# Kernel optimization log

Hardware: AMD Instinct MI355X
Metric: run time of the kernel (lower is better)

Reference implementation:

```python
import jax, jax.numpy as jnp
import numpy as np

B, IN, H, NC = 8192, 1024, 1024, 16
CS = H // NC  # chunk_size = 64


def cumsoftmax(x):
    # cumulative softmax along last dim
    return jnp.cumsum(jax.nn.softmax(x, axis=-1), axis=-1)


def setup_inputs() -> dict:
    key = jax.random.key(0)
    ks = jax.random.split(key, 9)
    s_ih = 1.0 / np.sqrt(IN)
    s_hh = 1.0 / np.sqrt(H)
    return {
        "x": jax.random.normal(ks[0], (B, IN), jnp.float32),
        "hx": jax.random.normal(ks[1], (B, H), jnp.float32),
        "cx": jax.random.normal(ks[2], (B, NC, CS), jnp.float32),
        "input_floor": jax.random.normal(ks[3], (B, NC), jnp.float32),
        "forget_floor": jax.random.normal(ks[4], (B, NC), jnp.float32),
        "W_ih": jax.random.uniform(ks[5], (4 * H, IN), jnp.float32, -s_ih, s_ih),
        "b_ih": jax.random.uniform(ks[6], (4 * H,), jnp.float32, -s_ih, s_ih),
        "W_hh": jax.random.uniform(ks[7], (4 * H, H), jnp.float32, -s_hh, s_hh),
        "b_hh": jax.random.uniform(ks[8], (4 * H,), jnp.float32, -s_hh, s_hh),
    }


def reference(x, hx, cx, input_floor, forget_floor, W_ih, b_ih, W_hh, b_hh):
    # dual GEMM (eval path: dropconnect=0.0 -> plain linear)
    gates = x @ W_ih.T + b_ih + hx @ W_hh.T + b_hh          # [B, 4H]
    g = gates.reshape(-1, NC * 4, CS)                        # [B, 4*NC, CS]
    outgate, cell, ingate, forgetgate = jnp.split(g, 4, axis=1)  # each [B, NC, CS]

    happy_in, sad_in = jnp.split(input_floor, 2, axis=1)     # [B, NC/2] each
    happy_fg, sad_fg = jnp.split(forget_floor, 2, axis=1)

    happy_cingate = cumsoftmax(happy_in)
    happy_cforgetgate = jnp.flip(cumsoftmax(jnp.flip(happy_fg, 1)), 1)
    sad_cingate = jnp.flip(cumsoftmax(jnp.flip(sad_in, 1)), 1)
    sad_cforgetgate = cumsoftmax(sad_fg)

    cingate = jnp.concatenate([happy_cingate, sad_cingate], axis=1)[:, :, None]      # [B, NC, 1]
    cforgetgate = jnp.concatenate([happy_cforgetgate, sad_cforgetgate], axis=1)[:, :, None]

    ingate = jax.nn.sigmoid(ingate)
    forgetgate = jax.nn.sigmoid(forgetgate)
    cell = jnp.tanh(cell)
    outgate = jax.nn.sigmoid(outgate)

    overlap = cforgetgate * cingate
    forgetgate = forgetgate * overlap + (cforgetgate - overlap)
    ingate = ingate * overlap + (cingate - overlap)

    cy = forgetgate * cx + ingate * cell                     # [B, NC, CS]
    hy = outgate * jnp.tanh(cy)
    return hy.reshape(-1, H), cy
```

## Files before the change

kernel.cpp:

```cpp
#include <hip/hip_runtime.h>
#include <hip/hip_bf16.h>


#define B_ROWS 8192
#define IN_DIM 1024
#define H_DIM  1024
#define NCHUNK 16
#define K_TOT  2048

#define BM   256
#define BN   256
#define BK   64
#define NKT  (K_TOT / BK)
#define THREADS 512

#define A_PACK_BYTES ((size_t)B_ROWS * K_TOT * 2)
#define W_PACK_BYTES ((size_t)16 * 256 * K_TOT * 2)

typedef __attribute__((ext_vector_type(4))) float  f32x4;
typedef __bf16 bf16x8 __attribute__((ext_vector_type(8)));

__device__ __forceinline__ float sigmoidf_(float x) {
    return 1.0f / (1.0f + __expf(-x));
}
__device__ __forceinline__ float tanhf_(float x) {
    float e = __expf(-2.0f * fabsf(x));
    float t = (1.0f - e) / (1.0f + e);
    return copysignf(t, x);
}

__device__ __forceinline__ void gload16(const __bf16* gsrc, __bf16* lds_dst) {
    __builtin_amdgcn_global_load_lds(
        (const __attribute__((address_space(1))) unsigned int*)gsrc,
        (__attribute__((address_space(3))) unsigned int*)lds_dst, 16, 0, 0);
}

__device__ __forceinline__ bf16x8 cvt8(f32x4 v0, f32x4 v1) {
    bf16x8 o;
    o[0] = (__bf16)v0.x; o[1] = (__bf16)v0.y; o[2] = (__bf16)v0.z; o[3] = (__bf16)v0.w;
    o[4] = (__bf16)v1.x; o[5] = (__bf16)v1.y; o[6] = (__bf16)v1.z; o[7] = (__bf16)v1.w;
    return o;
}

__global__ __launch_bounds__(256)
void pack_AW(const float* __restrict__ x, const float* __restrict__ hx,
             const float* __restrict__ W_ih, const float* __restrict__ W_hh,
             __bf16* __restrict__ Abf, __bf16* __restrict__ Wp)
{
    const int bid = blockIdx.x;
    const int c8  = threadIdx.x << 3;
    if (bid < B_ROWS) {
        const float* src = (c8 < IN_DIM)
            ? (x  + (size_t)bid * IN_DIM + c8)
            : (hx + (size_t)bid * IN_DIM + (c8 - IN_DIM));
        f32x4 v0 = *reinterpret_cast<const f32x4*>(src);
        f32x4 v1 = *reinterpret_cast<const f32x4*>(src + 4);
        *reinterpret_cast<bf16x8*>(Abf + (size_t)bid * K_TOT + c8) = cvt8(v0, v1);
    } else {
        const int r  = bid - B_ROWS;
        const int bh = r >> 8;
        const int n  = r & 255;
        const int g  = (n >> 4) & 3;
        const int j  = (n >> 6) * 16 + (n & 15);
        const int wr = g * H_DIM + bh * 64 + j;
        const float* src = (c8 < IN_DIM)
            ? (W_ih + (size_t)wr * IN_DIM + c8)
            : (W_hh + (size_t)wr * IN_DIM + (c8 - IN_DIM));
        f32x4 v0 = *reinterpret_cast<const f32x4*>(src);
        f32x4 v1 = *reinterpret_cast<const f32x4*>(src + 4);
        *reinterpret_cast<bf16x8*>(Wp + (size_t)r * K_TOT + c8) = cvt8(v0, v1);
    }
}

__device__ __forceinline__ void stage_half(const __bf16* __restrict__ gbase, int kb,
                                           __bf16* lbase, int row0, int tid) {
    #pragma unroll
    for (int i = 0; i < 2; ++i) {
        int e   = i * 4096 + tid * 8;
        int row = row0 + (e >> 6);
        int kd  = e & 63;
        gload16(gbase + (size_t)row * K_TOT + kb + (kd ^ ((row & 7) << 3)), lbase + e);
    }
}

#define SWZ(r, k) ((r) * 64 + ((k) ^ (((r) & 7) << 3)))

#define LDB(Bs) { \
    _Pragma("unroll") \
    for (int fn = 0; fn < 4; ++fn) { \
        int br = wcol + fn * 16 + lr; \
        bfr[fn][0] = *reinterpret_cast<const bf16x8*>(&(Bs)[SWZ(br, lh * 8)]); \
        bfr[fn][1] = *reinterpret_cast<const bf16x8*>(&(Bs)[SWZ(br, 32 + lh * 8)]); \
    } }

#define LDA(As, q) { \
    int ar = wrow + (q) * 32 + lr; \
    af[0][0] = *reinterpret_cast<const bf16x8*>(&(As)[SWZ(ar, lh * 8)]); \
    af[0][1] = *reinterpret_cast<const bf16x8*>(&(As)[SWZ(ar, 32 + lh * 8)]); \
    af[1][0] = *reinterpret_cast<const bf16x8*>(&(As)[SWZ(ar + 16, lh * 8)]); \
    af[1][1] = *reinterpret_cast<const bf16x8*>(&(As)[SWZ(ar + 16, 32 + lh * 8)]); \
    }

#define SB0 __builtin_amdgcn_sched_barrier(0)
#define LGKM0 asm volatile("s_waitcnt lgkmcnt(0)" ::: "memory")
#define BARRIER do { \
    asm volatile("" ::: "memory"); \
    __builtin_amdgcn_s_barrier(); \
    asm volatile("" ::: "memory"); \
} while (0)

#define MF(q) { \
    __builtin_amdgcn_s_setprio(1); \
    _Pragma("unroll") \
    for (int ks = 0; ks < 2; ++ks) { \
        _Pragma("unroll") \
        for (int fn = 0; fn < 4; ++fn) { \
            acc[2*(q)][fn]   = __builtin_amdgcn_mfma_f32_16x16x32_bf16(af[0][ks], bfr[fn][ks], acc[2*(q)][fn],   0,0,0); \
            acc[2*(q)+1][fn] = __builtin_amdgcn_mfma_f32_16x16x32_bf16(af[1][ks], bfr[fn][ks], acc[2*(q)+1][fn], 0,0,0); \
        } \
    } \
    __builtin_amdgcn_s_setprio(0); \
}

#define TILE(T, Ac, An2) { \
    const int t_ = (T); \
     \
    LDB(Bp); LDA(Ac, 0); \
    SB0; MF(0); LGKM0; BARRIER; \
     \
    LDA(Ac, 1); \
    stage_half(Wblk, ((t_ + 1) & 31) * BK, Bp,        0,   tid); \
    stage_half(Wblk, ((t_ + 1) & 31) * BK, Bp + 8192, 128, tid); \
    SB0; MF(1); SB0; \
     \
    LDA(Ac, 2); \
    stage_half(Arow, ((t_ + 2) & 31) * BK, An2,        0,   tid); \
    stage_half(Arow, ((t_ + 2) & 31) * BK, An2 + 8192, 128, tid); \
    SB0; MF(2); SB0; \
     \
    LDA(Ac, 3); \
    SB0; MF(3); LGKM0; \
    asm volatile("s_waitcnt vmcnt(4)" ::: "memory"); \
    BARRIER; \
}

__global__ __launch_bounds__(THREADS, 2)
void onlstm_gemm8(const __bf16* __restrict__ Abf, const __bf16* __restrict__ Wp,
                  const float* __restrict__ cx,
                  const float* __restrict__ input_floor,
                  const float* __restrict__ forget_floor,
                  const float* __restrict__ b_ih, const float* __restrict__ b_hh,
                  float* __restrict__ out)
{
    __shared__ __align__(16) __bf16 lds[65536];
    __shared__ float ci_s[BM], cf_s[BM], bias_s[BN];

    const int tid = threadIdx.x;
    const int n0  = blockIdx.x;
    const int bm  = (n0 & 7) * 4 + ((n0 >> 3) & 3);
    const int bh  = n0 >> 5;
    const int h0  = bh * 64;
    const int nc  = bh;

    if (tid < BM) {
        {
            int g = (tid >> 4) & 3;
            int j = (tid >> 6) * 16 + (tid & 15);
            int wrr = g * H_DIM + h0 + j;
            bias_s[tid] = b_ih[wrr] + b_hh[wrr];
        }
        int b = bm * BM + tid;
        const int off = (nc < 8) ? 0 : 8;
        const int ic  = (nc < 8) ? nc : (nc - 8);
        const float* pin = input_floor  + (size_t)b * NCHUNK + off;
        const float* pfg = forget_floor + (size_t)b * NCHUNK + off;
        float vi[8], vf[8];
        float mi = -1e30f, mf = -1e30f;
        #pragma unroll
        for (int t = 0; t < 8; ++t) {
            vi[t] = pin[t]; vf[t] = pfg[t];
            mi = fmaxf(mi, vi[t]); mf = fmaxf(mf, vf[t]);
        }
        float si = 0.f, sf = 0.f;
        #pragma unroll
        for (int t = 0; t < 8; ++t) {
            vi[t] = __expf(vi[t] - mi); vf[t] = __expf(vf[t] - mf);
            si += vi[t]; sf += vf[t];
        }
        float pi = 0.f, pf = 0.f;
        #pragma unroll
        for (int t = 0; t < 8; ++t) { if (t <= ic) { pi += vi[t]; pf += vf[t]; } }
        float suf_i = si - pi + vi[ic];
        float suf_f = sf - pf + vf[ic];
        float civ, cfv;
        if (nc < 8) { civ = pi / si;    cfv = suf_f / sf; }
        else        { civ = suf_i / si; cfv = pf / sf;    }
        ci_s[tid] = civ; cf_s[tid] = cfv;
    }

    const __bf16* Arow = Abf + (size_t)(bm * BM) * K_TOT;
    const __bf16* Wblk = Wp  + (size_t)bh * 256 * K_TOT;
    __bf16* const A0p = lds;
    __bf16* const A1p = lds + 16384;
    __bf16* const A2p = lds + 32768;
    __bf16* const Bp  = lds + 49152;

    stage_half(Arow, 0,  A0p,        0,   tid);
    stage_half(Arow, 0,  A0p + 8192, 128, tid);
    stage_half(Wblk, 0,  Bp,         0,   tid);
    stage_half(Wblk, 0,  Bp + 8192,  128, tid);
    stage_half(Arow, BK, A1p,        0,   tid);
    stage_half(Arow, BK, A1p + 8192, 128, tid);
    LGKM0;
    asm volatile("s_waitcnt vmcnt(4)" ::: "memory");
    __builtin_amdgcn_s_barrier();
    asm volatile("" ::: "memory");

    f32x4  acc[8][4];
    #pragma unroll
    for (int i = 0; i < 8; ++i)
        #pragma unroll
        for (int j = 0; j < 4; ++j) acc[i][j] = (f32x4){0.f, 0.f, 0.f, 0.f};
    bf16x8 af[2][2];
    bf16x8 bfr[4][2];

    const int l    = tid & 63;
    const int wid  = tid >> 6;
    const int wrw  = wid >> 2;
    const int wc   = wid & 3;
    const int lr   = l & 15;
    const int lh   = l >> 4;
    const int wrow = wrw * 128;
    const int wcol = wc * 64;

    #pragma unroll 1
    for (int it = 0; it < 10; ++it) {
        const int t = 3 * it;
        TILE(t,     A0p, A2p);
        TILE(t + 1, A1p, A0p);
        TILE(t + 2, A2p, A1p);
    }
    TILE(30, A0p, A2p);
    TILE(31, A1p, A0p);

    asm volatile("s_waitcnt vmcnt(0) lgkmcnt(0)" ::: "memory");
    __builtin_amdgcn_s_barrier();

    const size_t CY_OFF = (size_t)B_ROWS * H_DIM;
    const int hcol = h0 + wc * 16 + lr;
    #pragma unroll
    for (int m = 0; m < 8; ++m) {
        #pragma unroll
        for (int r = 0; r < 4; ++r) {
            int rt = wrow + m * 16 + lh * 4 + r;
            int b  = bm * BM + rt;
            float civ = ci_s[rt], cfv = cf_s[rt];
            float ovl = cfv * civ;
            float og = acc[m][0][r] + bias_s[wcol + lr];
            float cg = acc[m][1][r] + bias_s[wcol + 16 + lr];
            float ig = acc[m][2][r] + bias_s[wcol + 32 + lr];
            float fg = acc[m][3][r] + bias_s[wcol + 48 + lr];
            float i_s = sigmoidf_(ig);
            float f_s = sigmoidf_(fg);
            float c_t = tanhf_(cg);
            float o_s = sigmoidf_(og);
            float fq = f_s * ovl + (cfv - ovl);
            float iq = i_s * ovl + (civ - ovl);
            float cxv = cx[(size_t)b * H_DIM + hcol];
            float cyv = fq * cxv + iq * c_t;
            float hyv = o_s * tanhf_(cyv);
            out[(size_t)b * H_DIM + hcol] = hyv;
            out[CY_OFF + (size_t)b * H_DIM + hcol] = cyv;
        }
    }
}

extern "C" void kernel_launch(void* const* d_in, const int* in_sizes, int n_in,
                              void* d_out, int out_size, void* d_ws, size_t ws_size,
                              hipStream_t stream) {
    const float* x            = (const float*)d_in[0];
    const float* hx           = (const float*)d_in[1];
    const float* cx           = (const float*)d_in[2];
    const float* input_floor  = (const float*)d_in[3];
    const float* forget_floor = (const float*)d_in[4];
    const float* W_ih         = (const float*)d_in[5];
    const float* b_ih         = (const float*)d_in[6];
    const float* W_hh         = (const float*)d_in[7];
    const float* b_hh         = (const float*)d_in[8];
    float* out = (float*)d_out;

    __bf16* Abf = (__bf16*)d_ws;
    __bf16* Wp  = (__bf16*)((char*)d_ws + A_PACK_BYTES);
    pack_AW<<<B_ROWS + 16 * 256, 256, 0, stream>>>(x, hx, W_ih, W_hh, Abf, Wp);
    onlstm_gemm8<<<512, THREADS, 0, stream>>>(
        Abf, Wp, cx, input_floor, forget_floor, b_ih, b_hh, out);
}
```

Before: 162.8 us.

## Restructure GEMM main loop with double-buffered A/B LDS and register ping-pong

Replaces the triple-buffered A and single-buffered B LDS scheme with two A buffers and two B buffers. It also alternates two register sets for the A and B fragments, so the next tile's fragments are loaded from LDS while the current tile's MFMAs run. Global prefetch now runs one tile ahead for A and two ahead for B. The aim is to hide LDS read latency behind MFMA work and cut stalls at barriers. The cost is more register pressure at 2 blocks per CU, and the wait counts and barrier placement are delicate.

After: 207.3 us. 1.27x slower.

```diff
diff --git a/kernel.cpp b/kernel.cpp
--- a/kernel.cpp
+++ b/kernel.cpp
@@ -85,20 +85,20 @@
 
 #define SWZ(r, k) ((r) * 64 + ((k) ^ (((r) & 7) << 3)))
 
-#define LDB(Bs) { \
+#define LDB_TO(dst, Bs) { \
     _Pragma("unroll") \
     for (int fn = 0; fn < 4; ++fn) { \
         int br = wcol + fn * 16 + lr; \
-        bfr[fn][0] = *reinterpret_cast<const bf16x8*>(&(Bs)[SWZ(br, lh * 8)]); \
-        bfr[fn][1] = *reinterpret_cast<const bf16x8*>(&(Bs)[SWZ(br, 32 + lh * 8)]); \
+        dst[fn][0] = *reinterpret_cast<const bf16x8*>(&(Bs)[SWZ(br, lh * 8)]); \
+        dst[fn][1] = *reinterpret_cast<const bf16x8*>(&(Bs)[SWZ(br, 32 + lh * 8)]); \
     } }
 
-#define LDA(As, q) { \
+#define LDA_TO(dst, As, q) { \
     int ar = wrow + (q) * 32 + lr; \
-    af[0][0] = *reinterpret_cast<const bf16x8*>(&(As)[SWZ(ar, lh * 8)]); \
-    af[0][1] = *reinterpret_cast<const bf16x8*>(&(As)[SWZ(ar, 32 + lh * 8)]); \
-    af[1][0] = *reinterpret_cast<const bf16x8*>(&(As)[SWZ(ar + 16, lh * 8)]); \
-    af[1][1] = *reinterpret_cast<const bf16x8*>(&(As)[SWZ(ar + 16, 32 + lh * 8)]); \
+    dst[0][0] = *reinterpret_cast<const bf16x8*>(&(As)[SWZ(ar, lh * 8)]); \
+    dst[0][1] = *reinterpret_cast<const bf16x8*>(&(As)[SWZ(ar, 32 + lh * 8)]); \
+    dst[1][0] = *reinterpret_cast<const bf16x8*>(&(As)[SWZ(ar + 16, lh * 8)]); \
+    dst[1][1] = *reinterpret_cast<const bf16x8*>(&(As)[SWZ(ar + 16, 32 + lh * 8)]); \
     }
 
 #define SB0 __builtin_amdgcn_sched_barrier(0)
@@ -109,43 +109,45 @@
     asm volatile("" ::: "memory"); \
 } while (0)
 
-#define MF(q) { \
+#define MF_Q(q, a, b) { \
     __builtin_amdgcn_s_setprio(1); \
     _Pragma("unroll") \
     for (int ks = 0; ks < 2; ++ks) { \
         _Pragma("unroll") \
         for (int fn = 0; fn < 4; ++fn) { \
-            acc[2*(q)][fn]   = __builtin_amdgcn_mfma_f32_16x16x32_bf16(af[0][ks], bfr[fn][ks], acc[2*(q)][fn],   0,0,0); \
-            acc[2*(q)+1][fn] = __builtin_amdgcn_mfma_f32_16x16x32_bf16(af[1][ks], bfr[fn][ks], acc[2*(q)+1][fn], 0,0,0); \
+            acc[2*(q)][fn]   = __builtin_amdgcn_mfma_f32_16x16x32_bf16(a[0][ks], b[fn][ks], acc[2*(q)][fn],   0,0,0); \
+            acc[2*(q)+1][fn] = __builtin_amdgcn_mfma_f32_16x16x32_bf16(a[1][ks], b[fn][ks], acc[2*(q)+1][fn], 0,0,0); \
         } \
     } \
     __builtin_amdgcn_s_setprio(0); \
 }
 
-#define TILE(T, Ac, An2) { \
+#define TILE9(T, Ac, An, Bcur, Bnext, bcur, bnext) { \
     const int t_ = (T); \
      \
-    LDB(Bp); LDA(Ac, 0); \
-    SB0; MF(0); LGKM0; BARRIER; \
-     \
-    LDA(Ac, 1); \
-    stage_half(Wblk, ((t_ + 1) & 31) * BK, Bp,        0,   tid); \
-    stage_half(Wblk, ((t_ + 1) & 31) * BK, Bp + 8192, 128, tid); \
-    SB0; MF(1); SB0; \
-     \
-    LDA(Ac, 2); \
-    stage_half(Arow, ((t_ + 2) & 31) * BK, An2,        0,   tid); \
-    stage_half(Arow, ((t_ + 2) & 31) * BK, An2 + 8192, 128, tid); \
-    SB0; MF(2); SB0; \
-     \
-    LDA(Ac, 3); \
-    SB0; MF(3); LGKM0; \
+    stage_half(Arow, ((t_ + 1) & 31) * BK, An,        0,   tid); \
+    stage_half(Arow, ((t_ + 1) & 31) * BK, An + 8192, 128, tid); \
+    LDA_TO(afB, Ac, 1); \
+    SB0; MF_Q(0, afA, bcur); LGKM0; BARRIER; \
+     \
+    stage_half(Wblk, ((t_ + 2) & 31) * BK, Bcur,        0,   tid); \
+    LDA_TO(afA, Ac, 2); \
+    SB0; MF_Q(1, afB, bcur); SB0; \
+     \
+    stage_half(Wblk, ((t_ + 2) & 31) * BK, Bcur + 8192, 128, tid); \
+    LDA_TO(afB, Ac, 3); \
+    SB0; MF_Q(2, afA, bcur); SB0; \
+     \
     asm volatile("s_waitcnt vmcnt(4)" ::: "memory"); \
     BARRIER; \
+     \
+    LDB_TO(bnext, Bnext); \
+    LDA_TO(afA, An, 0); \
+    SB0; MF_Q(3, afB, bcur); LGKM0; BARRIER; \
 }
 
 __global__ __launch_bounds__(THREADS, 2)
-void onlstm_gemm8(const __bf16* __restrict__ Abf, const __bf16* __restrict__ Wp,
+void onlstm_gemm9(const __bf16* __restrict__ Abf, const __bf16* __restrict__ Wp,
                   const float* __restrict__ cx,
                   const float* __restrict__ input_floor,
                   const float* __restrict__ forget_floor,
@@ -202,27 +204,8 @@
     const __bf16* Wblk = Wp  + (size_t)bh * 256 * K_TOT;
     __bf16* const A0p = lds;
     __bf16* const A1p = lds + 16384;
-    __bf16* const A2p = lds + 32768;
-    __bf16* const Bp  = lds + 49152;
-
-    stage_half(Arow, 0,  A0p,        0,   tid);
-    stage_half(Arow, 0,  A0p + 8192, 128, tid);
-    stage_half(Wblk, 0,  Bp,         0,   tid);
-    stage_half(Wblk, 0,  Bp + 8192,  128, tid);
-    stage_half(Arow, BK, A1p,        0,   tid);
-    stage_half(Arow, BK, A1p + 8192, 128, tid);
-    LGKM0;
-    asm volatile("s_waitcnt vmcnt(4)" ::: "memory");
-    __builtin_amdgcn_s_barrier();
-    asm volatile("" ::: "memory");
-
-    f32x4  acc[8][4];
-    #pragma unroll
-    for (int i = 0; i < 8; ++i)
-        #pragma unroll
-        for (int j = 0; j < 4; ++j) acc[i][j] = (f32x4){0.f, 0.f, 0.f, 0.f};
-    bf16x8 af[2][2];
-    bf16x8 bfr[4][2];
+    __bf16* const B0p = lds + 32768;
+    __bf16* const B1p = lds + 49152;
 
     const int l    = tid & 63;
     const int wid  = tid >> 6;
@@ -233,16 +216,33 @@
     const int wrow = wrw * 128;
     const int wcol = wc * 64;
 
+    f32x4  acc[8][4];
+    #pragma unroll
+    for (int i = 0; i < 8; ++i)
+        #pragma unroll
+        for (int j = 0; j < 4; ++j) acc[i][j] = (f32x4){0.f, 0.f, 0.f, 0.f};
+    bf16x8 afA[2][2], afB[2][2];
+    bf16x8 bfrE[4][2], bfrO[4][2];
+
+    stage_half(Wblk, 0,  B0p,        0,   tid);
+    stage_half(Wblk, 0,  B0p + 8192, 128, tid);
+    stage_half(Arow, 0,  A0p,        0,   tid);
+    stage_half(Arow, 0,  A0p + 8192, 128, tid);
+    LGKM0;
+    asm volatile("s_waitcnt vmcnt(0)" ::: "memory");
+    __builtin_amdgcn_s_barrier();
+    asm volatile("" ::: "memory");
+    stage_half(Wblk, BK, B1p,        0,   tid);
+    stage_half(Wblk, BK, B1p + 8192, 128, tid);
+    LDB_TO(bfrE, B0p);
+    LDA_TO(afA, A0p, 0);
+
     #pragma unroll 1
-    for (int it = 0; it < 10; ++it) {
-        const int t = 3 * it;
-        TILE(t,     A0p, A2p);
-        TILE(t + 1, A1p, A0p);
-        TILE(t + 2, A2p, A1p);
-    }
-    TILE(30, A0p, A2p);
-    TILE(31, A1p, A0p);
-
+    for (int it = 0; it < NKT / 2; ++it) {
+        const int t = 2 * it;
+        TILE9(t,     A0p, A1p, B0p, B1p, bfrE, bfrO);
+        TILE9(t + 1, A1p, A0p, B1p, B0p, bfrO, bfrE);
+    }
     asm volatile("s_waitcnt vmcnt(0) lgkmcnt(0)" ::: "memory");
     __builtin_amdgcn_s_barrier();
 
@@ -292,6 +292,6 @@
     __bf16* Abf = (__bf16*)d_ws;
     __bf16* Wp  = (__bf16*)((char*)d_ws + A_PACK_BYTES);
     pack_AW<<<B_ROWS + 16 * 256, 256, 0, stream>>>(x, hx, W_ih, W_hh, Abf, Wp);
-    onlstm_gemm8<<<512, THREADS, 0, stream>>>(
+    onlstm_gemm9<<<512, THREADS, 0, stream>>>(
         Abf, Wp, cx, input_floor, forget_floor, b_ih, b_hh, out);
 }
```
